# Optimization experiments

Measured on AMD Instinct MI355X. Metric: run time of the kernel, lower is better.

Reference implementation:

```python
import jax, jax.numpy as jnp
import numpy as np

N, D, DB, E, H = 1024, 512, 64, 32768, 1024

def setup_inputs() -> dict:
    key = jax.random.key(0)
    k = jax.random.split(key, 6)
    object_feats = jax.random.normal(k[0], (N, D), dtype=jnp.float32)
    bboxes_embedding = jax.random.normal(k[1], (N, N, DB), dtype=jnp.float32)
    pairs = jax.random.randint(k[2], (E, 2), 0, N, dtype=jnp.int64)
    # Kaiming-normal-ish init for the two Linear layers
    W1 = jax.random.normal(k[3], (D + D + DB, H), dtype=jnp.float32) * np.sqrt(2.0 / (D + D + DB))
    b1 = jnp.zeros((H,), dtype=jnp.float32)
    W2 = jax.random.normal(k[4], (H, D), dtype=jnp.float32) * np.sqrt(2.0 / H)
    b2 = jnp.zeros((D,), dtype=jnp.float32)
    return {"object_feats": object_feats, "bboxes_embedding": bboxes_embedding,
            "pairs": pairs, "W1": W1, "b1": b1, "W2": W2, "b2": b2}

def reference(object_feats, bboxes_embedding, pairs, W1, b1, W2, b2):
    sub = pairs[:, 0]
    obj = pairs[:, 1]
    # gather pair features: [E, D] each, plus pairwise bbox embedding [E, DB]
    f_sub = object_feats[sub]
    f_obj = object_feats[obj]
    bb = bboxes_embedding[sub, obj]
    x = jnp.concatenate((f_sub, f_obj, bb), axis=1)  # [E, 2D+DB]
    h = jax.nn.relu(x @ W1 + b1)
    out = h @ W2 + b2  # [E, D]
    n = object_feats.shape[0]
    # scatter-mean into subject nodes; each node's own feature is included once,
    # so new_feat[i] = (object_feats[i] + sum_{pairs with sub==i} out) / (1 + count[i]).
    # Nodes with no incident pairs keep their original feature (count==0 -> identity).
    seg_sum = jax.ops.segment_sum(out, sub, num_segments=n)  # [N, D]
    count = jax.ops.segment_sum(jnp.ones((out.shape[0],), dtype=out.dtype), sub, num_segments=n)
    new_feats = (object_feats + seg_sum) / (1.0 + count)[:, None]
    return (new_feats, bboxes_embedding, pairs)
```

## Files before the change

kernel.cpp:

```cpp
#include <hip/hip_runtime.h>

#define N_OBJ 1024
#define E_P   32768

typedef float f32x4 __attribute__((ext_vector_type(4)));
typedef short bf16x8 __attribute__((ext_vector_type(8)));
typedef unsigned short u16x4 __attribute__((ext_vector_type(4)));

__device__ __forceinline__ unsigned short f2bf(float f) {
    unsigned u = __float_as_uint(f);
    u = u + 0x7FFFu + ((u >> 16) & 1u);
    return (unsigned short)(u >> 16);
}

#define OFF_A    0
#define LEN_A    4194304
#define OFF_B    (OFF_A + LEN_A)
#define LEN_B    5242880
#define OFF_OUT  (OFF_B + LEN_B)
#define LEN_OUT  7340032

__device__ __forceinline__ void copy_role(const float4* __restrict__ src,
                                          float4* __restrict__ dst,
                                          int off, int len, int nb, int cb) {
    int stride = nb * 256;
    int i = off + cb * 256 + threadIdx.x;
    int end = off + len;
    for (; i + stride < end; i += 2 * stride) {
        float4 a = src[i];
        float4 b = src[i + stride];
        dst[i] = a;
        dst[i + stride] = b;
    }
    if (i < end) dst[i] = src[i];
}

__global__ __launch_bounds__(256) void k_a(const float* __restrict__ W1,
                                           const float* __restrict__ W2,
                                           const float* __restrict__ feats,
                                           const int* __restrict__ pairs,
                                           unsigned short* __restrict__ w1pqT,
                                           unsigned short* __restrict__ w1cT,
                                           unsigned short* __restrict__ w2T,
                                           unsigned short* __restrict__ featsb,
                                           float* __restrict__ out_pairs,
                                           int* __restrict__ counts,
                                           int* __restrict__ rank,
                                           const float4* __restrict__ csrc,
                                           float4* __restrict__ cdst) {
    int bid = blockIdx.x, tid = threadIdx.x;
    if ((bid % 3) == 2) { copy_role(csrc, cdst, OFF_A, LEN_A, 1056, bid / 3); return; }
    int job = (bid / 3) * 2 + (bid % 3);
    if (job >= 1856) {
        int i = (job - 1856) * 256 + tid;
        out_pairs[i] = (float)pairs[i];
        if (i < E_P) rank[i] = atomicAdd(&counts[pairs[2 * i]], 1);
        return;
    }
    if (job >= 1600) {
        int base = (job - 1600) * 2048 + tid * 8;
        float4 v0 = *(const float4*)&feats[base];
        float4 v1 = *(const float4*)&feats[base + 4];
        u16x4 o0 = { f2bf(v0.x), f2bf(v0.y), f2bf(v0.z), f2bf(v0.w) };
        u16x4 o1 = { f2bf(v1.x), f2bf(v1.y), f2bf(v1.z), f2bf(v1.w) };
        *(u16x4*)&featsb[base] = o0;
        *(u16x4*)&featsb[base + 4] = o1;
        return;
    }
    const float* in; unsigned short* out;
    int LDI, LDO, r0, c0, nbase, kbase;
    if (job < 1024) {
        r0 = (job >> 5) * 32; c0 = (job & 31) * 32;
        in = W1; LDI = 1024; out = w1pqT; LDO = 512;
        nbase = c0 + (r0 >= 512 ? 1024 : 0); kbase = r0 & 511;
    } else if (job < 1088) {
        int t = job - 1024; r0 = 1024 + (t >> 5) * 32; c0 = (t & 31) * 32;
        in = W1; LDI = 1024; out = w1cT; LDO = 64;
        nbase = c0; kbase = r0 - 1024;
    } else {
        int t = job - 1088; r0 = (t >> 4) * 32; c0 = (t & 15) * 32;
        in = W2; LDI = 512; out = w2T; LDO = 1024;
        nbase = c0; kbase = r0;
    }
    __shared__ float lds[32][33];
    int ti = tid >> 3, tj = (tid & 7) * 4;
    float4 v = *(const float4*)&in[(size_t)(r0 + ti) * LDI + c0 + tj];
    lds[ti][tj] = v.x; lds[ti][tj + 1] = v.y; lds[ti][tj + 2] = v.z; lds[ti][tj + 3] = v.w;
    __syncthreads();
    int oc = tid >> 3, oj = (tid & 7) * 4;
    u16x4 o = { f2bf(lds[oj][oc]), f2bf(lds[oj + 1][oc]),
                f2bf(lds[oj + 2][oc]), f2bf(lds[oj + 3][oc]) };
    *(u16x4*)&out[(size_t)(nbase + oc) * LDO + kbase + oj] = o;
}

__global__ __launch_bounds__(256) void k_b(const int* __restrict__ counts,
                                           const int* __restrict__ rank,
                                           const int* __restrict__ pairs,
                                           int* __restrict__ csr_obj,
                                           unsigned* __restrict__ brec,
                                           int* __restrict__ bcnt,
                                           const unsigned short* __restrict__ featsb,
                                           const unsigned short* __restrict__ w1pqT,
                                           const float* __restrict__ b1,
                                           float* __restrict__ P, float* __restrict__ Q,
                                           const float4* __restrict__ csrc,
                                           float4* __restrict__ cdst) {
    int bid = blockIdx.x, tid = threadIdx.x;
    if ((bid % 3) < 2) { copy_role(csrc, cdst, OFF_B, LEN_B, 1282, (bid / 3) * 2 + (bid % 3)); return; }
    int role = bid / 3;

    if (role >= 129) {
        int job = role - 129;
        int m0 = (job >> 5) * 64, n0 = (job & 31) * 64;
        int w = tid >> 6, l = tid & 63;
        int ln = l & 15, kb = (l >> 4) * 8;
        int row = m0 + w * 16 + ln;
        f32x4 acc[4] = {};
        for (int k0 = 0; k0 < 512; k0 += 32) {
            bf16x8 a = *(const bf16x8*)&featsb[(size_t)row * 512 + k0 + kb];
            #pragma unroll
            for (int f = 0; f < 4; ++f) {
                bf16x8 b = *(const bf16x8*)&w1pqT[(size_t)(n0 + f * 16 + ln) * 512 + k0 + kb];
                acc[f] = __builtin_amdgcn_mfma_f32_16x16x32_bf16(a, b, acc[f], 0, 0, 0);
            }
        }
        int mr = m0 + w * 16 + (l >> 4) * 4;
        if (n0 < 1024) {
            #pragma unroll
            for (int f = 0; f < 4; ++f) {
                int n = n0 + f * 16 + ln;
                float b1v = b1[n];
                #pragma unroll
                for (int r = 0; r < 4; ++r)
                    P[(size_t)(mr + r) * 1024 + n] = acc[f][r] + b1v;
            }
        } else {
            #pragma unroll
            for (int f = 0; f < 4; ++f) {
                int n = n0 - 1024 + f * 16 + ln;
                #pragma unroll
                for (int r = 0; r < 4; ++r)
                    Q[(size_t)(mr + r) * 1024 + n] = acc[f][r];
            }
        }
        return;
    }

    __shared__ int sbuf[2][256];
    __shared__ int soff[1024];
    int c[4]; int s = 0;
    #pragma unroll
    for (int i = 0; i < 4; ++i) { c[i] = counts[tid * 4 + i]; s += c[i]; }
    sbuf[0][tid] = s;
    __syncthreads();
    int sel = 0;
    for (int d = 1; d < 256; d <<= 1) {
        int v = sbuf[sel][tid];
        if (tid >= d) v += sbuf[sel][tid - d];
        sbuf[sel ^ 1][tid] = v;
        sel ^= 1;
        __syncthreads();
    }
    int base = sbuf[sel][tid] - s;
    int run = base;
    #pragma unroll
    for (int i = 0; i < 4; ++i) { soff[tid * 4 + i] = run; run += c[i]; }
    __syncthreads();

    if (role >= 1) {
        int e = (role - 1) * 256 + tid;
        int sub = pairs[2 * e];
        csr_obj[soff[sub] + rank[e]] = pairs[2 * e + 1];
        return;
    }

    int nb[4]; int t = 0;
    #pragma unroll
    for (int i = 0; i < 4; ++i) { nb[i] = (c[i] + 31) >> 5; t += nb[i]; }
    __syncthreads();
    sbuf[0][tid] = t;
    __syncthreads();
    sel = 0;
    for (int d = 1; d < 256; d <<= 1) {
        int v = sbuf[sel][tid];
        if (tid >= d) v += sbuf[sel][tid - d];
        sbuf[sel ^ 1][tid] = v;
        sel ^= 1;
        __syncthreads();
    }
    int bpos = sbuf[sel][tid] - t;
    int run2 = base;
    #pragma unroll
    for (int i = 0; i < 4; ++i) {
        int seg = tid * 4 + i;
        for (int k = 0; k < nb[i]; ++k) {
            int st = run2 + k * 32;
            int cnt = c[i] - k * 32; if (cnt > 32) cnt = 32;
            brec[bpos++] = (unsigned)st | ((unsigned)seg << 16) | ((unsigned)(cnt - 1) << 26);
        }
        run2 += c[i];
    }
    if (tid == 255) bcnt[0] = bpos;
}

__global__ __launch_bounds__(256) void k_seg(const int* __restrict__ csr_obj,
                                             const unsigned* __restrict__ brec,
                                             const int* __restrict__ bcnt,
                                             const float* __restrict__ bb,
                                             const unsigned short* __restrict__ w1cT,
                                             const float* __restrict__ P,
                                             const float* __restrict__ Q,
                                             float* __restrict__ HS) {
    int b = blockIdx.x;
    if (b >= bcnt[0]) return;
    unsigned rec = brec[b];
    const int start = rec & 0xFFFF;
    const int seg = (rec >> 16) & 0x3FF;
    const int n = ((rec >> 26) & 31) + 1;

    const int tid = threadIdx.x, w = tid >> 6, l = tid & 63;
    const int ln = l & 15, g4 = l >> 4, kb = g4 * 8;
    const int n0 = w * 256;
    const int nA = n < 16 ? n : 16;
    const int nB = n - 16;

    int iA = start + (ln < nA ? ln : nA - 1);
    int iB = (nB > 0) ? (start + 16 + (ln < nB ? ln : nB - 1)) : iA;
    int objA = csr_obj[iA];
    int objB = csr_obj[iB];

    float pv[16];
    #pragma unroll
    for (int f = 0; f < 16; ++f)
        pv[f] = P[(size_t)seg * 1024 + n0 + f * 16 + ln];

    const float* brA = &bb[((size_t)seg * 1024 + (size_t)objA) * 64];
    const float* brB = &bb[((size_t)seg * 1024 + (size_t)objB) * 64];
    float4 a0 = *(const float4*)&brA[kb];
    float4 a1 = *(const float4*)&brA[kb + 4];
    float4 a2 = *(const float4*)&brA[32 + kb];
    float4 a3 = *(const float4*)&brA[32 + kb + 4];
    float4 c0 = *(const float4*)&brB[kb];
    float4 c1 = *(const float4*)&brB[kb + 4];
    float4 c2 = *(const float4*)&brB[32 + kb];
    float4 c3 = *(const float4*)&brB[32 + kb + 4];
    bf16x8 A0a, A1a, A0b, A1b;
    A0a[0] = (short)f2bf(a0.x); A0a[1] = (short)f2bf(a0.y); A0a[2] = (short)f2bf(a0.z); A0a[3] = (short)f2bf(a0.w);
    A0a[4] = (short)f2bf(a1.x); A0a[5] = (short)f2bf(a1.y); A0a[6] = (short)f2bf(a1.z); A0a[7] = (short)f2bf(a1.w);
    A1a[0] = (short)f2bf(a2.x); A1a[1] = (short)f2bf(a2.y); A1a[2] = (short)f2bf(a2.z); A1a[3] = (short)f2bf(a2.w);
    A1a[4] = (short)f2bf(a3.x); A1a[5] = (short)f2bf(a3.y); A1a[6] = (short)f2bf(a3.z); A1a[7] = (short)f2bf(a3.w);
    A0b[0] = (short)f2bf(c0.x); A0b[1] = (short)f2bf(c0.y); A0b[2] = (short)f2bf(c0.z); A0b[3] = (short)f2bf(c0.w);
    A0b[4] = (short)f2bf(c1.x); A0b[5] = (short)f2bf(c1.y); A0b[6] = (short)f2bf(c1.z); A0b[7] = (short)f2bf(c1.w);
    A1b[0] = (short)f2bf(c2.x); A1b[1] = (short)f2bf(c2.y); A1b[2] = (short)f2bf(c2.z); A1b[3] = (short)f2bf(c2.w);
    A1b[4] = (short)f2bf(c3.x); A1b[5] = (short)f2bf(c3.y); A1b[6] = (short)f2bf(c3.z); A1b[7] = (short)f2bf(c3.w);

    int raA0 = __shfl(objA, g4 * 4 + 0), raA1 = __shfl(objA, g4 * 4 + 1);
    int raA2 = __shfl(objA, g4 * 4 + 2), raA3 = __shfl(objA, g4 * 4 + 3);
    int raB0 = __shfl(objB, g4 * 4 + 0), raB1 = __shfl(objB, g4 * 4 + 1);
    int raB2 = __shfl(objB, g4 * 4 + 2), raB3 = __shfl(objB, g4 * 4 + 3);
    bool vA0 = (g4 * 4 + 0) < nA, vA1 = (g4 * 4 + 1) < nA;
    bool vA2 = (g4 * 4 + 2) < nA, vA3 = (g4 * 4 + 3) < nA;
    bool vB0 = (g4 * 4 + 0) < nB, vB1 = (g4 * 4 + 1) < nB;
    bool vB2 = (g4 * 4 + 2) < nB, vB3 = (g4 * 4 + 3) < nB;

    #pragma unroll 4
    for (int f = 0; f < 16; ++f) {
        int col = n0 + f * 16 + ln;
        const unsigned short* wr = &w1cT[(size_t)col * 64];
        bf16x8 b0 = *(const bf16x8*)&wr[kb];
        bf16x8 b1 = *(const bf16x8*)&wr[32 + kb];
        f32x4 dA = {0.f, 0.f, 0.f, 0.f};
        dA = __builtin_amdgcn_mfma_f32_16x16x32_bf16(A0a, b0, dA, 0, 0, 0);
        dA = __builtin_amdgcn_mfma_f32_16x16x32_bf16(A1a, b1, dA, 0, 0, 0);
        f32x4 dB = {0.f, 0.f, 0.f, 0.f};
        dB = __builtin_amdgcn_mfma_f32_16x16x32_bf16(A0b, b0, dB, 0, 0, 0);
        dB = __builtin_amdgcn_mfma_f32_16x16x32_bf16(A1b, b1, dB, 0, 0, 0);
        float qA0 = Q[(size_t)raA0 * 1024 + col];
        float qA1 = Q[(size_t)raA1 * 1024 + col];
        float qA2 = Q[(size_t)raA2 * 1024 + col];
        float qA3 = Q[(size_t)raA3 * 1024 + col];
        float qB0 = Q[(size_t)raB0 * 1024 + col];
        float qB1 = Q[(size_t)raB1 * 1024 + col];
        float qB2 = Q[(size_t)raB2 * 1024 + col];
        float qB3 = Q[(size_t)raB3 * 1024 + col];
        float h = 0.f;
        h += vA0 ? fmaxf(dA[0] + pv[f] + qA0, 0.f) : 0.f;
        h += vA1 ? fmaxf(dA[1] + pv[f] + qA1, 0.f) : 0.f;
        h += vA2 ? fmaxf(dA[2] + pv[f] + qA2, 0.f) : 0.f;
        h += vA3 ? fmaxf(dA[3] + pv[f] + qA3, 0.f) : 0.f;
        h += vB0 ? fmaxf(dB[0] + pv[f] + qB0, 0.f) : 0.f;
        h += vB1 ? fmaxf(dB[1] + pv[f] + qB1, 0.f) : 0.f;
        h += vB2 ? fmaxf(dB[2] + pv[f] + qB2, 0.f) : 0.f;
        h += vB3 ? fmaxf(dB[3] + pv[f] + qB3, 0.f) : 0.f;
        h += __shfl_xor(h, 16);
        h += __shfl_xor(h, 32);
        if (l < 16) atomicAdd(&HS[(size_t)seg * 1024 + n0 + f * 16 + l], h);
    }
}

__global__ __launch_bounds__(256) void k_out(const float* __restrict__ HS,
                                             const unsigned short* __restrict__ w2T,
                                             const float* __restrict__ feats,
                                             const float* __restrict__ b2,
                                             const int* __restrict__ counts,
                                             float* __restrict__ out0,
                                             const float4* __restrict__ csrc,
                                             float4* __restrict__ cdst) {
    int bid = blockIdx.x;
    if ((bid % 17) != 16) { copy_role(csrc, cdst, OFF_OUT, LEN_OUT, 2048, (bid / 17) * 16 + (bid % 17)); return; }
    int job = bid / 17;
    int m0 = (job >> 3) * 64, n0 = (job & 7) * 64;
    int tid = threadIdx.x, w = tid >> 6, l = tid & 63;
    int ln = l & 15, kb = (l >> 4) * 8;
    int row = m0 + w * 16 + ln;
    f32x4 acc[4] = {};
    for (int k0 = 0; k0 < 1024; k0 += 32) {
        const float* hp = &HS[(size_t)row * 1024 + k0 + kb];
        float4 h0 = *(const float4*)&hp[0];
        float4 h1 = *(const float4*)&hp[4];
        bf16x8 a;
        a[0] = (short)f2bf(h0.x); a[1] = (short)f2bf(h0.y); a[2] = (short)f2bf(h0.z); a[3] = (short)f2bf(h0.w);
        a[4] = (short)f2bf(h1.x); a[5] = (short)f2bf(h1.y); a[6] = (short)f2bf(h1.z); a[7] = (short)f2bf(h1.w);
        #pragma unroll
        for (int f = 0; f < 4; ++f) {
            bf16x8 b = *(const bf16x8*)&w2T[(size_t)(n0 + f * 16 + ln) * 1024 + k0 + kb];
            acc[f] = __builtin_amdgcn_mfma_f32_16x16x32_bf16(a, b, acc[f], 0, 0, 0);
        }
    }
    int mr = m0 + w * 16 + (l >> 4) * 4;
    float cv[4], inv[4];
    #pragma unroll
    for (int r = 0; r < 4; ++r) {
        float c = (float)counts[mr + r];
        cv[r] = c;
        inv[r] = 1.0f / (1.0f + c);
    }
    #pragma unroll
    for (int f = 0; f < 4; ++f) {
        int n = n0 + f * 16 + ln;
        float b2v = b2[n];
        #pragma unroll
        for (int r = 0; r < 4; ++r) {
            float fv = feats[(size_t)(mr + r) * 512 + n];
            out0[(size_t)(mr + r) * 512 + n] = (fv + acc[f][r] + cv[r] * b2v) * inv[r];
        }
    }
}

extern "C" void kernel_launch(void* const* d_in, const int* in_sizes, int n_in,
                              void* d_out, int out_size, void* d_ws, size_t ws_size,
                              hipStream_t stream) {
    const float* feats = (const float*)d_in[0];
    const float* bb    = (const float*)d_in[1];
    const int*   pairs = (const int*)d_in[2];
    const float* W1    = (const float*)d_in[3];
    const float* b1    = (const float*)d_in[4];
    const float* W2    = (const float*)d_in[5];
    const float* b2    = (const float*)d_in[6];

    float* out        = (float*)d_out;
    float* out_feats  = out;
    float* out_bb     = out + (size_t)N_OBJ * 512;
    float* out_pairs  = out + (size_t)N_OBJ * 512 + (size_t)N_OBJ * N_OBJ * 64;

    char* w = (char*)d_ws;
    unsigned short* featsb = (unsigned short*)w;
    unsigned short* w1pqT  = (unsigned short*)(w + (1u << 20));
    float*          HS     = (float*)w;
    unsigned short* w1cT   = (unsigned short*)(w + (4u << 20));
    unsigned short* w2T    = (unsigned short*)(w + (4u << 20) + (128u << 10));
    float* P = (float*)(w + (5u << 20) + (128u << 10));
    float* Q = (float*)(w + (9u << 20) + (128u << 10));
    char* ints = w + (13u << 20) + (128u << 10);
    int*      counts  = (int*)ints;
    int*      csr_obj = (int*)(ints + 4096);
    unsigned* brec    = (unsigned*)(ints + 4096 + 131072);
    int*      bcnt    = (int*)(ints + 4096 + 131072 + 16384);
    int*      rank    = (int*)(ints + 4096 + 131072 + 16384 + 64);

    const float4* cbb  = (const float4*)bb;
    float4*       cobb = (float4*)out_bb;

    hipMemsetAsync(counts, 0, 4096, stream);

    k_a<<<3168, 256, 0, stream>>>(W1, W2, feats, pairs, w1pqT, w1cT, w2T, featsb,
                                  out_pairs, counts, rank, cbb, cobb);
    k_b<<<1923, 256, 0, stream>>>(counts, rank, pairs, csr_obj, brec, bcnt,
                                  featsb, w1pqT, b1, P, Q, cbb, cobb);

    hipMemsetAsync(HS, 0, (size_t)N_OBJ * 1024 * sizeof(float), stream);

    k_seg<<<2048, 256, 0, stream>>>(csr_obj, brec, bcnt, bb, w1cT, P, Q, HS);
    k_out<<<2176, 256, 0, stream>>>(HS, w2T, feats, b2, counts, out_feats, cbb, cobb);
}
```

Before: 233.2 us.

## Split segment kernel into column quarters, stage Q rows in LDS, overlap bbox copy

Each k_seg work record is now split across four blocks, one per 256-column quarter. Every block stages the 32 gathered Q rows for its quarter in shared memory with coalesced float4 loads, replacing the scattered per-lane global Q reads. One in five blocks instead copies a slice of the bboxes passthrough, so the copy work is rebalanced from the other kernels into k_seg. This adds a barrier and 32KB of LDS per block, and the 4x4 bbox tile loads plus MFMA operand setup are now repeated once per quarter.

```diff
diff --git a/kernel.cpp b/kernel.cpp
--- a/kernel.cpp
+++ b/kernel.cpp
@@ -14,11 +14,13 @@
 }
 
 #define OFF_A    0
-#define LEN_A    4194304
+#define LEN_A    3670016
 #define OFF_B    (OFF_A + LEN_A)
-#define LEN_B    5242880
-#define OFF_OUT  (OFF_B + LEN_B)
-#define LEN_OUT  7340032
+#define LEN_B    4194304
+#define OFF_SEG  (OFF_B + LEN_B)
+#define LEN_SEG  4194304
+#define OFF_OUT  (OFF_SEG + LEN_SEG)
+#define LEN_OUT  4718592
 
 __device__ __forceinline__ void copy_role(const float4* __restrict__ src,
                                           float4* __restrict__ dst,
@@ -210,8 +212,13 @@
                                              const unsigned short* __restrict__ w1cT,
                                              const float* __restrict__ P,
                                              const float* __restrict__ Q,
-                                             float* __restrict__ HS) {
-    int b = blockIdx.x;
+                                             float* __restrict__ HS,
+                                             const float4* __restrict__ csrc,
+                                             float4* __restrict__ cdst) {
+    int bid = blockIdx.x;
+    if ((bid % 5) == 4) { copy_role(csrc, cdst, OFF_SEG, LEN_SEG, 2048, bid / 5); return; }
+    int job = (bid / 5) * 4 + (bid % 5);
+    int b = job >> 2, qd = job & 3;
     if (b >= bcnt[0]) return;
     unsigned rec = brec[b];
     const int start = rec & 0xFFFF;
@@ -220,19 +227,28 @@
 
     const int tid = threadIdx.x, w = tid >> 6, l = tid & 63;
     const int ln = l & 15, g4 = l >> 4, kb = g4 * 8;
-    const int n0 = w * 256;
+    const int cbase = qd * 256;
+    const int wbase = cbase + w * 64;
+
+    __shared__ float qs[32][256];
+
+    {
+        int p = tid >> 3, j = tid & 7;
+        int op = csr_obj[start + (p < n ? p : n - 1)];
+        const float* qrow = &Q[(size_t)op * 1024 + cbase];
+        #pragma unroll
+        for (int i = 0; i < 8; ++i) {
+            int c = j * 4 + i * 32;
+            *(float4*)&qs[p][c] = *(const float4*)&qrow[c];
+        }
+    }
+
     const int nA = n < 16 ? n : 16;
     const int nB = n - 16;
-
     int iA = start + (ln < nA ? ln : nA - 1);
     int iB = (nB > 0) ? (start + 16 + (ln < nB ? ln : nB - 1)) : iA;
     int objA = csr_obj[iA];
     int objB = csr_obj[iB];
-
-    float pv[16];
-    #pragma unroll
-    for (int f = 0; f < 16; ++f)
-        pv[f] = P[(size_t)seg * 1024 + n0 + f * 16 + ln];
 
     const float* brA = &bb[((size_t)seg * 1024 + (size_t)objA) * 64];
     const float* brB = &bb[((size_t)seg * 1024 + (size_t)objB) * 64];
@@ -254,18 +270,22 @@
     A1b[0] = (short)f2bf(c2.x); A1b[1] = (short)f2bf(c2.y); A1b[2] = (short)f2bf(c2.z); A1b[3] = (short)f2bf(c2.w);
     A1b[4] = (short)f2bf(c3.x); A1b[5] = (short)f2bf(c3.y); A1b[6] = (short)f2bf(c3.z); A1b[7] = (short)f2bf(c3.w);
 
-    int raA0 = __shfl(objA, g4 * 4 + 0), raA1 = __shfl(objA, g4 * 4 + 1);
-    int raA2 = __shfl(objA, g4 * 4 + 2), raA3 = __shfl(objA, g4 * 4 + 3);
-    int raB0 = __shfl(objB, g4 * 4 + 0), raB1 = __shfl(objB, g4 * 4 + 1);
-    int raB2 = __shfl(objB, g4 * 4 + 2), raB3 = __shfl(objB, g4 * 4 + 3);
     bool vA0 = (g4 * 4 + 0) < nA, vA1 = (g4 * 4 + 1) < nA;
     bool vA2 = (g4 * 4 + 2) < nA, vA3 = (g4 * 4 + 3) < nA;
     bool vB0 = (g4 * 4 + 0) < nB, vB1 = (g4 * 4 + 1) < nB;
     bool vB2 = (g4 * 4 + 2) < nB, vB3 = (g4 * 4 + 3) < nB;
 
-    #pragma unroll 4
-    for (int f = 0; f < 16; ++f) {
-        int col = n0 + f * 16 + ln;
+    float pv[4];
+    #pragma unroll
+    for (int f = 0; f < 4; ++f)
+        pv[f] = P[(size_t)seg * 1024 + wbase + f * 16 + ln];
+
+    __syncthreads();
+
+    #pragma unroll
+    for (int f = 0; f < 4; ++f) {
+        int col = wbase + f * 16 + ln;
+        int cc = col - cbase;
         const unsigned short* wr = &w1cT[(size_t)col * 64];
         bf16x8 b0 = *(const bf16x8*)&wr[kb];
         bf16x8 b1 = *(const bf16x8*)&wr[32 + kb];
@@ -275,14 +295,14 @@
         f32x4 dB = {0.f, 0.f, 0.f, 0.f};
         dB = __builtin_amdgcn_mfma_f32_16x16x32_bf16(A0b, b0, dB, 0, 0, 0);
         dB = __builtin_amdgcn_mfma_f32_16x16x32_bf16(A1b, b1, dB, 0, 0, 0);
-        float qA0 = Q[(size_t)raA0 * 1024 + col];
-        float qA1 = Q[(size_t)raA1 * 1024 + col];
-        float qA2 = Q[(size_t)raA2 * 1024 + col];
-        float qA3 = Q[(size_t)raA3 * 1024 + col];
-        float qB0 = Q[(size_t)raB0 * 1024 + col];
-        float qB1 = Q[(size_t)raB1 * 1024 + col];
-        float qB2 = Q[(size_t)raB2 * 1024 + col];
-        float qB3 = Q[(size_t)raB3 * 1024 + col];
+        float qA0 = qs[g4 * 4 + 0][cc];
+        float qA1 = qs[g4 * 4 + 1][cc];
+        float qA2 = qs[g4 * 4 + 2][cc];
+        float qA3 = qs[g4 * 4 + 3][cc];
+        float qB0 = qs[16 + g4 * 4 + 0][cc];
+        float qB1 = qs[16 + g4 * 4 + 1][cc];
+        float qB2 = qs[16 + g4 * 4 + 2][cc];
+        float qB3 = qs[16 + g4 * 4 + 3][cc];
         float h = 0.f;
         h += vA0 ? fmaxf(dA[0] + pv[f] + qA0, 0.f) : 0.f;
         h += vA1 ? fmaxf(dA[1] + pv[f] + qA1, 0.f) : 0.f;
@@ -294,7 +314,7 @@
         h += vB3 ? fmaxf(dB[3] + pv[f] + qB3, 0.f) : 0.f;
         h += __shfl_xor(h, 16);
         h += __shfl_xor(h, 32);
-        if (l < 16) atomicAdd(&HS[(size_t)seg * 1024 + n0 + f * 16 + l], h);
+        if (l < 16) atomicAdd(&HS[(size_t)seg * 1024 + wbase + f * 16 + l], h);
     }
 }
 
@@ -390,6 +410,6 @@
 
     hipMemsetAsync(HS, 0, (size_t)N_OBJ * 1024 * sizeof(float), stream);
 
-    k_seg<<<2048, 256, 0, stream>>>(csr_obj, brec, bcnt, bb, w1cT, P, Q, HS);
+    k_seg<<<10240, 256, 0, stream>>>(csr_obj, brec, bcnt, bb, w1cT, P, Q, HS, cbb, cobb);
     k_out<<<2176, 256, 0, stream>>>(HS, w2T, feats, b2, counts, out_feats, cbb, cobb);
 }
```

New measurement: 231.5 us. About the same (-0.7%).
